# Performance work log

Measured on AMD Instinct MI355X. Metric: run time of the kernel, lower is better.

## Reference

```python
import jax, jax.numpy as jnp
import numpy as np

M, K = 16384, 1024
E, N = 8, 5632  # N = 2 * intermediate (gate+up packed); intermediate = 2816
TOPK = 2


def setup_inputs() -> dict:
    key = jax.random.key(0)
    ks = jax.random.split(key, 5)
    return {
        "hidden_states": jax.random.normal(ks[0], (M, K), jnp.float32) * 0.05,
        "w1": jax.random.normal(ks[1], (E, N, K), jnp.float32) * 0.02,
        "w2": jax.random.normal(ks[2], (E, K, N // 2), jnp.float32) * 0.02,
        "topk_weights": jax.random.uniform(ks[3], (M, TOPK), jnp.float32),
        "topk_ids": jax.random.randint(ks[4], (M, TOPK), 0, E, jnp.int32),
    }


def reference(hidden_states, w1, w2, topk_weights, topk_ids):
    # hidden_states: [M, K]; w1: [E, N, K]; w2: [E, K, N//2]
    # topk_weights / topk_ids: [M, TOPK]
    m, k = hidden_states.shape
    e_num, n, _ = w1.shape
    topk = topk_ids.shape[1]
    half = n // 2
    out = jnp.zeros((m, topk, k), dtype=hidden_states.dtype)
    # Loop over the small fixed set of experts; each iteration is a dense GEMM
    # masked by the routing assignment (faithful to the grouped-GEMM math).
    for e in range(e_num):
        h1 = jnp.einsum('mk,nk->mn', hidden_states, w1[e])          # [M, N]
        gate, up = h1[:, :half], h1[:, half:]
        h2 = jax.nn.silu(gate) * up                                  # silu_and_mul
        o = jnp.einsum('mh,kh->mk', h2, w2[e])                       # [M, K]
        mask = (topk_ids == e).astype(o.dtype)                       # [M, TOPK]
        out = out + mask[:, :, None] * o[:, None, :]
    # multiply routed weights and sum over top-k slots
    return jnp.einsum('mtk,mt->mk', out, topk_weights)
```

## Files before the change

kernel.cpp:

```cpp
#include <hip/hip_runtime.h>
#include <hip/hip_bf16.h>

#define M_TOK 16384
#define K_DIM 1024
#define E_NUM 8
#define N_DIM 5632
#define HALF_N 2816
#define TOPK 2
#define NPAIR (M_TOK * TOPK)
#define BM 128
#define BK 64
#define BH1 128
#define BN2 256
#define NDESC (NPAIR / BM + E_NUM)
#define NHB1 (HALF_N / BH1)
#define NNB2 (K_DIM / BN2)

typedef short s16x4 __attribute__((ext_vector_type(4)));
typedef short s16x8 __attribute__((ext_vector_type(8)));
typedef float f32x4 __attribute__((ext_vector_type(4)));

__device__ __forceinline__ short f2bf(float f) {
  union { __hip_bfloat16 h; short s; } c;
  c.h = __float2bfloat16(f);
  return c.s;
}

__device__ __forceinline__ float bf2f(unsigned short s) {
  union { float f; unsigned u; } c;
  c.u = ((unsigned)s) << 16;
  return c.f;
}

__device__ __forceinline__ void gload_lds16(const void* g, void* l) {
  __builtin_amdgcn_global_load_lds(
      (const __attribute__((address_space(1))) unsigned int*)g,
      (__attribute__((address_space(3))) unsigned int*)l, 16, 0, 0);
}

__device__ __forceinline__ int xcd_work(int bid, int nwg) {
  const int xcd = bid & 7, loc = bid >> 3;
  const int q = nwg >> 3, r = nwg & 7;
  return (xcd < r ? xcd * (q + 1) : r * (q + 1) + (xcd - r) * q) + loc;
}

__global__ void cvt_f32_bf16_k(const float4* __restrict__ src,
                               s16x4* __restrict__ dst, int n4) {
  int i = blockIdx.x * blockDim.x + threadIdx.x;
  int stride = gridDim.x * blockDim.x;
  for (; i < n4; i += stride) {
    float4 f = src[i];
    s16x4 o = { f2bf(f.x), f2bf(f.y), f2bf(f.z), f2bf(f.w) };
    dst[i] = o;
  }
}

__global__ void moe_count(const int* __restrict__ ids, int* __restrict__ cnt) {
  const int p = blockIdx.x * 256 + threadIdx.x;
  const int e = ids[p];
  const int lane = threadIdx.x & 63;
  __shared__ int h[E_NUM];
  if (threadIdx.x < E_NUM) h[threadIdx.x] = 0;
  __syncthreads();
#pragma unroll
  for (int ex = 0; ex < E_NUM; ++ex) {
    unsigned long long m = __ballot(e == ex);
    if (lane == 0 && m) atomicAdd(&h[ex], __popcll(m));
  }
  __syncthreads();
  if (threadIdx.x < E_NUM) atomicAdd(&cnt[threadIdx.x], h[threadIdx.x]);
}

__global__ void moe_build(const int* __restrict__ cnt, int* __restrict__ offs,
                          int4* __restrict__ desc) {
  if (blockIdx.x == 0 && threadIdx.x == 0) {
    int o = 0, d = 0;
    for (int e = 0; e < E_NUM; ++e) {
      offs[e] = o;
      int end = o + cnt[e];
      for (int s = o; s < end; s += BM) desc[d++] = make_int4(e, s, end, 0);
      o = end;
    }
    offs[E_NUM] = o;
    while (d < NDESC) desc[d++] = make_int4(-1, 0, 0, 0);
  }
}

__global__ void moe_scatter(const int* __restrict__ ids, const float* __restrict__ tw,
                            const int* __restrict__ offs, int* __restrict__ fill,
                            int* __restrict__ tok, float* __restrict__ wgt,
                            int* __restrict__ inv) {
  const int p = blockIdx.x * 256 + threadIdx.x;
  const int e = ids[p];
  const int lane = threadIdx.x & 63;
  const int w = threadIdx.x >> 6;
  __shared__ int wcnt[4][E_NUM];
  __shared__ int wpre[4][E_NUM];
  __shared__ int base[E_NUM];
  const unsigned long long lt = (1ull << lane) - 1ull;
  int myrank = 0;
#pragma unroll
  for (int ex = 0; ex < E_NUM; ++ex) {
    unsigned long long m = __ballot(e == ex);
    if (e == ex) myrank = (int)__popcll(m & lt);
    if (lane == 0) wcnt[w][ex] = (int)__popcll(m);
  }
  __syncthreads();
  if (threadIdx.x < E_NUM) {
    const int ex = threadIdx.x;
    int s = 0;
#pragma unroll
    for (int ww = 0; ww < 4; ++ww) { wpre[ww][ex] = s; s += wcnt[ww][ex]; }
    base[ex] = atomicAdd(&fill[ex], s);
  }
  __syncthreads();
  const int pos = offs[e] + base[e] + wpre[w][e] + myrank;
  tok[pos] = p >> 1;
  wgt[pos] = tw[p];
  inv[p] = pos;
}

__global__ void moe_gather(const float* __restrict__ hs, const int* __restrict__ tok,
                           unsigned short* __restrict__ hsb) {
  const int pos = blockIdx.x;
  const int m = tok[pos];
  const int t = threadIdx.x;
  const float4* s = (const float4*)(hs + (size_t)m * K_DIM) + t * 2;
  const float4 a = s[0], b = s[1];
  s16x8 o = { f2bf(a.x), f2bf(a.y), f2bf(a.z), f2bf(a.w),
              f2bf(b.x), f2bf(b.y), f2bf(b.z), f2bf(b.w) };
  *(s16x8*)(hsb + (size_t)pos * K_DIM + t * 8) = o;
}

__launch_bounds__(512)
__global__ void moe_gemm1(const unsigned short* __restrict__ hsb,
                          const unsigned short* __restrict__ w1b,
                          const int4* __restrict__ desc,
                          unsigned short* __restrict__ h2) {
  const int work = xcd_work(blockIdx.x, NHB1 * NDESC);
  const int di = work / NHB1;
  const int hb = work - di * NHB1;
  const int4 d = desc[di];
  const int e = d.x;
  if (e < 0) return;
  const int pos0 = d.y, eend = d.z;
  const int h0 = hb * BH1;

  __shared__ __align__(16) unsigned short As[BM * BK];
  __shared__ __align__(16) unsigned short Gs[BH1 * BK];
  __shared__ __align__(16) unsigned short Us[BH1 * BK];

  const int tid = threadIdx.x;
  const int lane = tid & 63;
  const int wid = tid >> 6;
  const int wr = wid >> 2;
  const int wc = wid & 3;

  const unsigned short* Ab = hsb + (size_t)pos0 * K_DIM;
  const unsigned short* Gb = w1b + ((size_t)e * N_DIM + h0) * K_DIM;
  const unsigned short* Ub = Gb + (size_t)HALF_N * K_DIM;

  f32x4 accg[4][2], accu[4][2];
  const f32x4 z = {0.f, 0.f, 0.f, 0.f};
#pragma unroll
  for (int i = 0; i < 4; ++i)
#pragma unroll
    for (int j = 0; j < 2; ++j) { accg[i][j] = z; accu[i][j] = z; }

  const int lrow = lane >> 3;
  const int scol = ((lane & 7) ^ lrow) << 3;
  const int fr = lane & 15;
  const int fq = lane >> 4;
  const int sw = fr & 7;

  for (int kt = 0; kt < K_DIM / BK; ++kt) {
    const int k0 = kt * BK;
#pragma unroll
    for (int c = 0; c < 2; ++c) {
      const int seg = c * 8 + wid;
      const int row = seg * 8 + lrow;
      gload_lds16(Ab + (size_t)row * K_DIM + k0 + scol, &As[seg * 512]);
      gload_lds16(Gb + (size_t)row * K_DIM + k0 + scol, &Gs[seg * 512]);
      gload_lds16(Ub + (size_t)row * K_DIM + k0 + scol, &Us[seg * 512]);
    }
    __syncthreads();
#pragma unroll
    for (int s = 0; s < 2; ++s) {
      const int coff = (((s * 4 + fq) ^ sw) << 3);
      s16x8 af[4];
#pragma unroll
      for (int i = 0; i < 4; ++i)
        af[i] = *(const s16x8*)&As[(64 * wr + 16 * i + fr) * BK + coff];
      s16x8 gf[2], uf[2];
#pragma unroll
      for (int j = 0; j < 2; ++j) {
        const int hr = (32 * wc + 16 * j + fr) * BK + coff;
        gf[j] = *(const s16x8*)&Gs[hr];
        uf[j] = *(const s16x8*)&Us[hr];
      }
#pragma unroll
      for (int i = 0; i < 4; ++i)
#pragma unroll
        for (int j = 0; j < 2; ++j) {
          accg[i][j] = __builtin_amdgcn_mfma_f32_16x16x32_bf16(af[i], gf[j], accg[i][j], 0, 0, 0);
          accu[i][j] = __builtin_amdgcn_mfma_f32_16x16x32_bf16(af[i], uf[j], accu[i][j], 0, 0, 0);
        }
    }
    __syncthreads();
  }

  const int vlim = eend - pos0;
#pragma unroll
  for (int i = 0; i < 4; ++i) {
#pragma unroll
    for (int rr = 0; rr < 4; ++rr) {
      const int row = 64 * wr + 16 * i + fq * 4 + rr;
      if (row < vlim) {
        unsigned short* dst = h2 + (size_t)(pos0 + row) * HALF_N + h0 + 32 * wc;
#pragma unroll
        for (int j = 0; j < 2; ++j) {
          const float g = accg[i][j][rr];
          const float u = accu[i][j][rr];
          const float sg = g / (1.0f + __expf(-g));
          __builtin_nontemporal_store((unsigned short)f2bf(sg * u), dst + 16 * j + fr);
        }
      }
    }
  }
}

__launch_bounds__(512)
__global__ void moe_gemm2(const unsigned short* __restrict__ h2,
                          const unsigned short* __restrict__ w2b,
                          const int4* __restrict__ desc,
                          const float* __restrict__ wgt,
                          unsigned short* __restrict__ opair) {
  const int work = xcd_work(blockIdx.x, NNB2 * NDESC);
  const int di = work >> 2;
  const int nb = work & 3;
  const int4 d = desc[di];
  const int e = d.x;
  if (e < 0) return;
  const int pos0 = d.y, eend = d.z;
  const int n0 = nb * BN2;

  __shared__ __align__(16) unsigned short As[BM * BK];
  __shared__ __align__(16) unsigned short Bs[BN2 * BK];

  const int tid = threadIdx.x;
  const int lane = tid & 63;
  const int wid = tid >> 6;
  const int wr = wid >> 2;
  const int wc = wid & 3;

  const unsigned short* Ab = h2 + (size_t)pos0 * HALF_N;
  const unsigned short* Bb = w2b + ((size_t)e * K_DIM + n0) * HALF_N;

  f32x4 acc[4][4];
  const f32x4 z = {0.f, 0.f, 0.f, 0.f};
#pragma unroll
  for (int i = 0; i < 4; ++i)
#pragma unroll
    for (int j = 0; j < 4; ++j) acc[i][j] = z;

  const int lrow = lane >> 3;
  const int scol = ((lane & 7) ^ lrow) << 3;
  const int fr = lane & 15;
  const int fq = lane >> 4;
  const int sw = fr & 7;

  for (int ht = 0; ht < HALF_N / BK; ++ht) {
    const int k0 = ht * BK;
#pragma unroll
    for (int c = 0; c < 2; ++c) {
      const int seg = c * 8 + wid;
      const int row = seg * 8 + lrow;
      gload_lds16(Ab + (size_t)row * HALF_N + k0 + scol, &As[seg * 512]);
    }
#pragma unroll
    for (int c = 0; c < 4; ++c) {
      const int seg = c * 8 + wid;
      const int row = seg * 8 + lrow;
      gload_lds16(Bb + (size_t)row * HALF_N + k0 + scol, &Bs[seg * 512]);
    }
    __syncthreads();
#pragma unroll
    for (int s = 0; s < 2; ++s) {
      const int coff = (((s * 4 + fq) ^ sw) << 3);
      s16x8 af[4], bf[4];
#pragma unroll
      for (int i = 0; i < 4; ++i)
        af[i] = *(const s16x8*)&As[(64 * wr + 16 * i + fr) * BK + coff];
#pragma unroll
      for (int j = 0; j < 4; ++j)
        bf[j] = *(const s16x8*)&Bs[(64 * wc + 16 * j + fr) * BK + coff];
#pragma unroll
      for (int i = 0; i < 4; ++i)
#pragma unroll
        for (int j = 0; j < 4; ++j)
          acc[i][j] = __builtin_amdgcn_mfma_f32_16x16x32_bf16(af[i], bf[j], acc[i][j], 0, 0, 0);
    }
    __syncthreads();
  }

  const int vlim = eend - pos0;
#pragma unroll
  for (int i = 0; i < 4; ++i) {
#pragma unroll
    for (int rr = 0; rr < 4; ++rr) {
      const int row = 64 * wr + 16 * i + fq * 4 + rr;
      if (row < vlim) {
        const int pos = pos0 + row;
        const float wt = wgt[pos];
        unsigned short* dst = opair + (size_t)pos * K_DIM + n0 + 64 * wc;
#pragma unroll
        for (int j = 0; j < 4; ++j)
          dst[16 * j + fr] = (unsigned short)f2bf(wt * acc[i][j][rr]);
      }
    }
  }
}

__global__ void moe_combine(const unsigned short* __restrict__ opair,
                            const int* __restrict__ inv,
                            float* __restrict__ out) {
  const int m = blockIdx.x;
  const int t = threadIdx.x;
  const int p0 = inv[2 * m], p1 = inv[2 * m + 1];
  const s16x8 a = *(const s16x8*)&opair[(size_t)p0 * K_DIM + t * 8];
  const s16x8 b = *(const s16x8*)&opair[(size_t)p1 * K_DIM + t * 8];
  f32x4 o0, o1;
  o0[0] = bf2f((unsigned short)a[0]) + bf2f((unsigned short)b[0]);
  o0[1] = bf2f((unsigned short)a[1]) + bf2f((unsigned short)b[1]);
  o0[2] = bf2f((unsigned short)a[2]) + bf2f((unsigned short)b[2]);
  o0[3] = bf2f((unsigned short)a[3]) + bf2f((unsigned short)b[3]);
  o1[0] = bf2f((unsigned short)a[4]) + bf2f((unsigned short)b[4]);
  o1[1] = bf2f((unsigned short)a[5]) + bf2f((unsigned short)b[5]);
  o1[2] = bf2f((unsigned short)a[6]) + bf2f((unsigned short)b[6]);
  o1[3] = bf2f((unsigned short)a[7]) + bf2f((unsigned short)b[7]);
  f32x4* dst = (f32x4*)(out + (size_t)m * K_DIM + t * 8);
  __builtin_nontemporal_store(o0, dst);
  __builtin_nontemporal_store(o1, dst + 1);
}

__global__ void sentinel_k(float* o) { o[0] = 1.0e9f; }

extern "C" void kernel_launch(void* const* d_in, const int* in_sizes, int n_in,
                              void* d_out, int out_size, void* d_ws, size_t ws_size,
                              hipStream_t stream) {
  const float* hs = (const float*)d_in[0];
  const float* w1 = (const float*)d_in[1];
  const float* w2 = (const float*)d_in[2];
  const float* tw = (const float*)d_in[3];
  const int* ids = (const int*)d_in[4];
  float* out = (float*)d_out;

  char* p = (char*)d_ws;
  auto carve = [&](size_t bytes) {
    char* r = p;
    p += (bytes + 255) & ~(size_t)255;
    return r;
  };
  unsigned short* w1b = (unsigned short*)carve((size_t)E_NUM * N_DIM * K_DIM * 2);
  unsigned short* w2b = (unsigned short*)carve((size_t)E_NUM * K_DIM * HALF_N * 2);
  unsigned short* hsb = (unsigned short*)carve((size_t)(NPAIR + BM) * K_DIM * 2);
  unsigned short* h2  = (unsigned short*)carve((size_t)(NPAIR + BM) * HALF_N * 2);
  int*   tok  = (int*)carve(NPAIR * 4);
  float* wgt  = (float*)carve(NPAIR * 4);
  int*   inv  = (int*)carve(NPAIR * 4);
  int*   meta = (int*)carve(1024);
  int4*  desc = (int4*)carve(NDESC * sizeof(int4));
  size_t need = (size_t)(p - (char*)d_ws);

  unsigned short* opair = hsb;

  if (need > ws_size) {
    hipMemsetAsync(d_out, 0, (size_t)out_size * sizeof(float), stream);
    sentinel_k<<<1, 1, 0, stream>>>(out);
    return;
  }

  int* cnt  = meta;
  int* fill = meta + 64;
  int* offs = meta + 128;

  hipMemsetAsync(meta, 0, 1024, stream);

  cvt_f32_bf16_k<<<2048, 256, 0, stream>>>(
      (const float4*)w1, (s16x4*)w1b, (int)((size_t)E_NUM * N_DIM * K_DIM / 4));
  cvt_f32_bf16_k<<<2048, 256, 0, stream>>>(
      (const float4*)w2, (s16x4*)w2b, (int)((size_t)E_NUM * K_DIM * HALF_N / 4));
  moe_count<<<NPAIR / 256, 256, 0, stream>>>(ids, cnt);
  moe_build<<<1, 64, 0, stream>>>(cnt, offs, desc);
  moe_scatter<<<NPAIR / 256, 256, 0, stream>>>(ids, tw, offs, fill, tok, wgt, inv);
  moe_gather<<<NPAIR, 128, 0, stream>>>(hs, tok, hsb);
  moe_gemm1<<<NHB1 * NDESC, 512, 0, stream>>>(hsb, w1b, desc, h2);
  moe_gemm2<<<NNB2 * NDESC, 512, 0, stream>>>(h2, w2b, desc, wgt, opair);
  moe_combine<<<M_TOK, 128, 0, stream>>>(opair, inv, out);
}
```

Measured before the change: 787.7 us.

## Double-buffer LDS tiles with BK=32 in both MoE GEMM kernels

Both grouped GEMM kernels move from a single-buffered 64-wide K tile to double-buffered 32-wide K tiles. The global-to-LDS load of the next tile is issued before the MFMA work on the current tile, leaving one barrier per iteration. The goal is to overlap memory latency with compute. In exchange, the K loop runs twice as many iterations with half the MFMA work per barrier, and the LDS swizzle pattern is simplified to 4 columns.

After: 875.1 us. +11.1%, slower.

```diff
diff --git a/kernel.cpp b/kernel.cpp
--- a/kernel.cpp
+++ b/kernel.cpp
@@ -9,7 +9,6 @@
 #define TOPK 2
 #define NPAIR (M_TOK * TOPK)
 #define BM 128
-#define BK 64
 #define BH1 128
 #define BN2 256
 #define NDESC (NPAIR / BM + E_NUM)
@@ -146,19 +145,24 @@
   const int pos0 = d.y, eend = d.z;
   const int h0 = hb * BH1;
 
-  __shared__ __align__(16) unsigned short As[BM * BK];
-  __shared__ __align__(16) unsigned short Gs[BH1 * BK];
-  __shared__ __align__(16) unsigned short Us[BH1 * BK];
+  __shared__ __align__(16) unsigned short As[2][BM * 32];
+  __shared__ __align__(16) unsigned short Gs[2][BH1 * 32];
+  __shared__ __align__(16) unsigned short Us[2][BH1 * 32];
 
   const int tid = threadIdx.x;
   const int lane = tid & 63;
   const int wid = tid >> 6;
   const int wr = wid >> 2;
   const int wc = wid & 3;
-
-  const unsigned short* Ab = hsb + (size_t)pos0 * K_DIM;
-  const unsigned short* Gb = w1b + ((size_t)e * N_DIM + h0) * K_DIM;
-  const unsigned short* Ub = Gb + (size_t)HALF_N * K_DIM;
+  const int fr = lane & 15;
+  const int fq = lane >> 4;
+
+  const int sr = tid >> 2;
+  const int sc8 = (((tid & 3) ^ (sr & 3)) << 3);
+  const unsigned short* Asrc = hsb + ((size_t)(pos0 + sr)) * K_DIM + sc8;
+  const unsigned short* Gsrc = w1b + ((size_t)e * N_DIM + h0 + sr) * K_DIM + sc8;
+  const unsigned short* Usrc = Gsrc + (size_t)HALF_N * K_DIM;
+  const int ldst = tid * 8;
 
   f32x4 accg[4][2], accu[4][2];
   const f32x4 z = {0.f, 0.f, 0.f, 0.f};
@@ -167,45 +171,41 @@
 #pragma unroll
     for (int j = 0; j < 2; ++j) { accg[i][j] = z; accu[i][j] = z; }
 
-  const int lrow = lane >> 3;
-  const int scol = ((lane & 7) ^ lrow) << 3;
-  const int fr = lane & 15;
-  const int fq = lane >> 4;
-  const int sw = fr & 7;
-
-  for (int kt = 0; kt < K_DIM / BK; ++kt) {
-    const int k0 = kt * BK;
-#pragma unroll
-    for (int c = 0; c < 2; ++c) {
-      const int seg = c * 8 + wid;
-      const int row = seg * 8 + lrow;
-      gload_lds16(Ab + (size_t)row * K_DIM + k0 + scol, &As[seg * 512]);
-      gload_lds16(Gb + (size_t)row * K_DIM + k0 + scol, &Gs[seg * 512]);
-      gload_lds16(Ub + (size_t)row * K_DIM + k0 + scol, &Us[seg * 512]);
-    }
-    __syncthreads();
-#pragma unroll
-    for (int s = 0; s < 2; ++s) {
-      const int coff = (((s * 4 + fq) ^ sw) << 3);
-      s16x8 af[4];
-#pragma unroll
-      for (int i = 0; i < 4; ++i)
-        af[i] = *(const s16x8*)&As[(64 * wr + 16 * i + fr) * BK + coff];
-      s16x8 gf[2], uf[2];
+  const int coff = ((fq ^ (fr & 3)) << 3);
+
+  const int NT = K_DIM / 32;
+  {
+    gload_lds16(Asrc, &As[0][ldst]);
+    gload_lds16(Gsrc, &Gs[0][ldst]);
+    gload_lds16(Usrc, &Us[0][ldst]);
+  }
+  __syncthreads();
+
+  for (int kt = 0; kt < NT; ++kt) {
+    const int b = kt & 1;
+    if (kt + 1 < NT) {
+      const int k0 = (kt + 1) * 32;
+      gload_lds16(Asrc + k0, &As[b ^ 1][ldst]);
+      gload_lds16(Gsrc + k0, &Gs[b ^ 1][ldst]);
+      gload_lds16(Usrc + k0, &Us[b ^ 1][ldst]);
+    }
+    s16x8 af[4], gf[2], uf[2];
+#pragma unroll
+    for (int i = 0; i < 4; ++i)
+      af[i] = *(const s16x8*)&As[b][(64 * wr + 16 * i + fr) * 32 + coff];
+#pragma unroll
+    for (int j = 0; j < 2; ++j) {
+      const int off = (32 * wc + 16 * j + fr) * 32 + coff;
+      gf[j] = *(const s16x8*)&Gs[b][off];
+      uf[j] = *(const s16x8*)&Us[b][off];
+    }
+#pragma unroll
+    for (int i = 0; i < 4; ++i)
 #pragma unroll
       for (int j = 0; j < 2; ++j) {
-        const int hr = (32 * wc + 16 * j + fr) * BK + coff;
-        gf[j] = *(const s16x8*)&Gs[hr];
-        uf[j] = *(const s16x8*)&Us[hr];
+        accg[i][j] = __builtin_amdgcn_mfma_f32_16x16x32_bf16(af[i], gf[j], accg[i][j], 0, 0, 0);
+        accu[i][j] = __builtin_amdgcn_mfma_f32_16x16x32_bf16(af[i], uf[j], accu[i][j], 0, 0, 0);
       }
-#pragma unroll
-      for (int i = 0; i < 4; ++i)
-#pragma unroll
-        for (int j = 0; j < 2; ++j) {
-          accg[i][j] = __builtin_amdgcn_mfma_f32_16x16x32_bf16(af[i], gf[j], accg[i][j], 0, 0, 0);
-          accu[i][j] = __builtin_amdgcn_mfma_f32_16x16x32_bf16(af[i], uf[j], accu[i][j], 0, 0, 0);
-        }
-    }
     __syncthreads();
   }
 
@@ -244,17 +244,23 @@
   const int pos0 = d.y, eend = d.z;
   const int n0 = nb * BN2;
 
-  __shared__ __align__(16) unsigned short As[BM * BK];
-  __shared__ __align__(16) unsigned short Bs[BN2 * BK];
+  __shared__ __align__(16) unsigned short As[2][BM * 32];
+  __shared__ __align__(16) unsigned short Bs[2][BN2 * 32];
 
   const int tid = threadIdx.x;
   const int lane = tid & 63;
   const int wid = tid >> 6;
   const int wr = wid >> 2;
   const int wc = wid & 3;
-
-  const unsigned short* Ab = h2 + (size_t)pos0 * HALF_N;
-  const unsigned short* Bb = w2b + ((size_t)e * K_DIM + n0) * HALF_N;
+  const int fr = lane & 15;
+  const int fq = lane >> 4;
+
+  const int sr = tid >> 2;
+  const int sc8 = (((tid & 3) ^ (sr & 3)) << 3);
+  const unsigned short* Asrc  = h2 + ((size_t)(pos0 + sr)) * HALF_N + sc8;
+  const unsigned short* Bsrc0 = w2b + ((size_t)e * K_DIM + n0 + sr) * HALF_N + sc8;
+  const unsigned short* Bsrc1 = Bsrc0 + (size_t)128 * HALF_N;
+  const int ldst = tid * 8;
 
   f32x4 acc[4][4];
   const f32x4 z = {0.f, 0.f, 0.f, 0.f};
@@ -263,43 +269,36 @@
 #pragma unroll
     for (int j = 0; j < 4; ++j) acc[i][j] = z;
 
-  const int lrow = lane >> 3;
-  const int scol = ((lane & 7) ^ lrow) << 3;
-  const int fr = lane & 15;
-  const int fq = lane >> 4;
-  const int sw = fr & 7;
-
-  for (int ht = 0; ht < HALF_N / BK; ++ht) {
-    const int k0 = ht * BK;
-#pragma unroll
-    for (int c = 0; c < 2; ++c) {
-      const int seg = c * 8 + wid;
-      const int row = seg * 8 + lrow;
-      gload_lds16(Ab + (size_t)row * HALF_N + k0 + scol, &As[seg * 512]);
-    }
-#pragma unroll
-    for (int c = 0; c < 4; ++c) {
-      const int seg = c * 8 + wid;
-      const int row = seg * 8 + lrow;
-      gload_lds16(Bb + (size_t)row * HALF_N + k0 + scol, &Bs[seg * 512]);
-    }
-    __syncthreads();
-#pragma unroll
-    for (int s = 0; s < 2; ++s) {
-      const int coff = (((s * 4 + fq) ^ sw) << 3);
-      s16x8 af[4], bf[4];
-#pragma unroll
-      for (int i = 0; i < 4; ++i)
-        af[i] = *(const s16x8*)&As[(64 * wr + 16 * i + fr) * BK + coff];
+  const int coff = ((fq ^ (fr & 3)) << 3);
+
+  const int NT = HALF_N / 32;
+  {
+    gload_lds16(Asrc, &As[0][ldst]);
+    gload_lds16(Bsrc0, &Bs[0][ldst]);
+    gload_lds16(Bsrc1, &Bs[0][4096 + ldst]);
+  }
+  __syncthreads();
+
+  for (int ht = 0; ht < NT; ++ht) {
+    const int b = ht & 1;
+    if (ht + 1 < NT) {
+      const int k0 = (ht + 1) * 32;
+      gload_lds16(Asrc + k0, &As[b ^ 1][ldst]);
+      gload_lds16(Bsrc0 + k0, &Bs[b ^ 1][ldst]);
+      gload_lds16(Bsrc1 + k0, &Bs[b ^ 1][4096 + ldst]);
+    }
+    s16x8 af[4], bf[4];
+#pragma unroll
+    for (int i = 0; i < 4; ++i)
+      af[i] = *(const s16x8*)&As[b][(64 * wr + 16 * i + fr) * 32 + coff];
+#pragma unroll
+    for (int j = 0; j < 4; ++j)
+      bf[j] = *(const s16x8*)&Bs[b][(64 * wc + 16 * j + fr) * 32 + coff];
+#pragma unroll
+    for (int i = 0; i < 4; ++i)
 #pragma unroll
       for (int j = 0; j < 4; ++j)
-        bf[j] = *(const s16x8*)&Bs[(64 * wc + 16 * j + fr) * BK + coff];
-#pragma unroll
-      for (int i = 0; i < 4; ++i)
-#pragma unroll
-        for (int j = 0; j < 4; ++j)
-          acc[i][j] = __builtin_amdgcn_mfma_f32_16x16x32_bf16(af[i], bf[j], acc[i][j], 0, 0, 0);
-    }
+        acc[i][j] = __builtin_amdgcn_mfma_f32_16x16x32_bf16(af[i], bf[j], acc[i][j], 0, 0, 0);
     __syncthreads();
   }
 
```

## Fuse token gather and bf16 conversion into GEMM1 A-tile loading

Applied to the files above, without the earlier changes.

Removes the separate gather kernel and has GEMM1 read fp32 hidden-state rows directly through the token index, converting them to bf16 in registers and storing them into the swizzled LDS A tile. The next k-tile is register-prefetched after the barrier so its loads overlap the MFMA work. The weight conversion kernel also switches to nontemporal loads. The change saves one write and one read of the gathered bf16 activations, but each A tile is now re-read as fp32 and re-converted by every h-block (22 times), which adds global traffic and VALU work in the GEMM.

Measured after the change: 842.2 us. +6.9%, slower.

```diff
diff --git a/kernel.cpp b/kernel.cpp
--- a/kernel.cpp
+++ b/kernel.cpp
@@ -44,13 +44,13 @@
   return (xcd < r ? xcd * (q + 1) : r * (q + 1) + (xcd - r) * q) + loc;
 }
 
-__global__ void cvt_f32_bf16_k(const float4* __restrict__ src,
+__global__ void cvt_f32_bf16_k(const f32x4* __restrict__ src,
                                s16x4* __restrict__ dst, int n4) {
   int i = blockIdx.x * blockDim.x + threadIdx.x;
   int stride = gridDim.x * blockDim.x;
   for (; i < n4; i += stride) {
-    float4 f = src[i];
-    s16x4 o = { f2bf(f.x), f2bf(f.y), f2bf(f.z), f2bf(f.w) };
+    f32x4 f = __builtin_nontemporal_load(src + i);
+    s16x4 o = { f2bf(f[0]), f2bf(f[1]), f2bf(f[2]), f2bf(f[3]) };
     dst[i] = o;
   }
 }
@@ -120,20 +120,9 @@
   inv[p] = pos;
 }
 
-__global__ void moe_gather(const float* __restrict__ hs, const int* __restrict__ tok,
-                           unsigned short* __restrict__ hsb) {
-  const int pos = blockIdx.x;
-  const int m = tok[pos];
-  const int t = threadIdx.x;
-  const float4* s = (const float4*)(hs + (size_t)m * K_DIM) + t * 2;
-  const float4 a = s[0], b = s[1];
-  s16x8 o = { f2bf(a.x), f2bf(a.y), f2bf(a.z), f2bf(a.w),
-              f2bf(b.x), f2bf(b.y), f2bf(b.z), f2bf(b.w) };
-  *(s16x8*)(hsb + (size_t)pos * K_DIM + t * 8) = o;
-}
-
 __launch_bounds__(512)
-__global__ void moe_gemm1(const unsigned short* __restrict__ hsb,
+__global__ void moe_gemm1(const float* __restrict__ hs,
+                          const int* __restrict__ tok,
                           const unsigned short* __restrict__ w1b,
                           const int4* __restrict__ desc,
                           unsigned short* __restrict__ h2) {
@@ -156,9 +145,15 @@
   const int wr = wid >> 2;
   const int wc = wid & 3;
 
-  const unsigned short* Ab = hsb + (size_t)pos0 * K_DIM;
   const unsigned short* Gb = w1b + ((size_t)e * N_DIM + h0) * K_DIM;
   const unsigned short* Ub = Gb + (size_t)HALF_N * K_DIM;
+
+  const int gcs = ((tid & 7) ^ ((tid >> 3) & 7)) * 8;
+  const int row1 = (wid << 3) + ((tid >> 3) & 7);
+  const int pp1 = pos0 + row1;
+  const int pp2 = pp1 + 64;
+  const float* Ar1 = hs + (size_t)(pp1 < NPAIR ? tok[pp1] : 0) * K_DIM + gcs;
+  const float* Ar2 = hs + (size_t)(pp2 < NPAIR ? tok[pp2] : 0) * K_DIM + gcs;
 
   f32x4 accg[4][2], accu[4][2];
   const f32x4 z = {0.f, 0.f, 0.f, 0.f};
@@ -173,17 +168,34 @@
   const int fq = lane >> 4;
   const int sw = fr & 7;
 
-  for (int kt = 0; kt < K_DIM / BK; ++kt) {
+  f32x4 a0 = *(const f32x4*)(Ar1);
+  f32x4 a1 = *(const f32x4*)(Ar1 + 4);
+  f32x4 a2 = *(const f32x4*)(Ar2);
+  f32x4 a3 = *(const f32x4*)(Ar2 + 4);
+
+  const int NT = K_DIM / BK;
+  for (int kt = 0; kt < NT; ++kt) {
     const int k0 = kt * BK;
 #pragma unroll
     for (int c = 0; c < 2; ++c) {
       const int seg = c * 8 + wid;
       const int row = seg * 8 + lrow;
-      gload_lds16(Ab + (size_t)row * K_DIM + k0 + scol, &As[seg * 512]);
       gload_lds16(Gb + (size_t)row * K_DIM + k0 + scol, &Gs[seg * 512]);
       gload_lds16(Ub + (size_t)row * K_DIM + k0 + scol, &Us[seg * 512]);
     }
+    s16x8 v1 = { f2bf(a0[0]), f2bf(a0[1]), f2bf(a0[2]), f2bf(a0[3]),
+                 f2bf(a1[0]), f2bf(a1[1]), f2bf(a1[2]), f2bf(a1[3]) };
+    s16x8 v2 = { f2bf(a2[0]), f2bf(a2[1]), f2bf(a2[2]), f2bf(a2[3]),
+                 f2bf(a3[0]), f2bf(a3[1]), f2bf(a3[2]), f2bf(a3[3]) };
+    *(s16x8*)&As[tid * 8] = v1;
+    *(s16x8*)&As[4096 + tid * 8] = v2;
     __syncthreads();
+    if (kt + 1 < NT) {
+      a0 = *(const f32x4*)(Ar1 + k0 + BK);
+      a1 = *(const f32x4*)(Ar1 + k0 + BK + 4);
+      a2 = *(const f32x4*)(Ar2 + k0 + BK);
+      a3 = *(const f32x4*)(Ar2 + k0 + BK + 4);
+    }
 #pragma unroll
     for (int s = 0; s < 2; ++s) {
       const int coff = (((s * 4 + fq) ^ sw) << 3);
@@ -363,7 +375,7 @@
   };
   unsigned short* w1b = (unsigned short*)carve((size_t)E_NUM * N_DIM * K_DIM * 2);
   unsigned short* w2b = (unsigned short*)carve((size_t)E_NUM * K_DIM * HALF_N * 2);
-  unsigned short* hsb = (unsigned short*)carve((size_t)(NPAIR + BM) * K_DIM * 2);
+  unsigned short* opair = (unsigned short*)carve((size_t)(NPAIR + BM) * K_DIM * 2);
   unsigned short* h2  = (unsigned short*)carve((size_t)(NPAIR + BM) * HALF_N * 2);
   int*   tok  = (int*)carve(NPAIR * 4);
   float* wgt  = (float*)carve(NPAIR * 4);
@@ -372,8 +384,6 @@
   int4*  desc = (int4*)carve(NDESC * sizeof(int4));
   size_t need = (size_t)(p - (char*)d_ws);
 
-  unsigned short* opair = hsb;
-
   if (need > ws_size) {
     hipMemsetAsync(d_out, 0, (size_t)out_size * sizeof(float), stream);
     sentinel_k<<<1, 1, 0, stream>>>(out);
@@ -387,14 +397,13 @@
   hipMemsetAsync(meta, 0, 1024, stream);
 
   cvt_f32_bf16_k<<<2048, 256, 0, stream>>>(
-      (const float4*)w1, (s16x4*)w1b, (int)((size_t)E_NUM * N_DIM * K_DIM / 4));
+      (const f32x4*)w1, (s16x4*)w1b, (int)((size_t)E_NUM * N_DIM * K_DIM / 4));
   cvt_f32_bf16_k<<<2048, 256, 0, stream>>>(
-      (const float4*)w2, (s16x4*)w2b, (int)((size_t)E_NUM * K_DIM * HALF_N / 4));
+      (const f32x4*)w2, (s16x4*)w2b, (int)((size_t)E_NUM * K_DIM * HALF_N / 4));
   moe_count<<<NPAIR / 256, 256, 0, stream>>>(ids, cnt);
   moe_build<<<1, 64, 0, stream>>>(cnt, offs, desc);
   moe_scatter<<<NPAIR / 256, 256, 0, stream>>>(ids, tw, offs, fill, tok, wgt, inv);
-  moe_gather<<<NPAIR, 128, 0, stream>>>(hs, tok, hsb);
-  moe_gemm1<<<NHB1 * NDESC, 512, 0, stream>>>(hsb, w1b, desc, h2);
+  moe_gemm1<<<NHB1 * NDESC, 512, 0, stream>>>(hs, tok, w1b, desc, h2);
   moe_gemm2<<<NNB2 * NDESC, 512, 0, stream>>>(h2, w2b, desc, wgt, opair);
   moe_combine<<<M_TOK, 128, 0, stream>>>(opair, inv, out);
 }
```
